# Performance work log

Hardware: AMD Instinct MI355X
Metric: run time of the kernel (lower is better)

Reference implementation:

```python
import jax, jax.numpy as jnp
import numpy as np

B, C1, C2, H, W = 8, 256, 256, 64, 64
C = 256            # int(c1*e)
G = C // 16        # 16 groups (dg)
Cg = C // G        # 16 channels per group
K = 9              # 3x3 kernel sample points
BN_EPS = 1e-5

# kernel grid offsets for 3x3, dilation 1 (pad=1 centers the grid)
KH = jnp.array([-1, -1, -1, 0, 0, 0, 1, 1, 1], jnp.float32)
KW = jnp.array([-1, 0, 1, -1, 0, 1, -1, 0, 1], jnp.float32)


def setup_inputs() -> dict:
    key = jax.random.key(0)
    ks = jax.random.split(key, 10)
    x = jax.random.normal(ks[0], (B, C1, H, W), jnp.float32)
    w_cv1 = jax.random.normal(ks[1], (C, C1), jnp.float32) / np.sqrt(C1)
    b_cv1 = jax.random.normal(ks[2], (C,), jnp.float32) * 0.1
    # offset/mask linear (DCNv4 inits to zero; small scale keeps sampling sane)
    w_off = jax.random.normal(ks[3], (G * 3 * K, C), jnp.float32) * 0.01
    b_off = jax.random.normal(ks[4], (G * 3 * K,), jnp.float32) * 0.01
    w_cv2 = jax.random.normal(ks[5], (C2, C), jnp.float32) / np.sqrt(C)
    bn_gamma = jax.random.uniform(ks[6], (C2,), jnp.float32, 0.5, 1.5)
    bn_beta = jax.random.normal(ks[7], (C2,), jnp.float32) * 0.1
    bn_mean = jax.random.normal(ks[8], (C2,), jnp.float32) * 0.1
    bn_var = jax.random.uniform(ks[9], (C2,), jnp.float32, 0.5, 1.5)
    return dict(x=x, w_cv1=w_cv1, b_cv1=b_cv1, w_off=w_off, b_off=b_off,
                w_cv2=w_cv2, bn_gamma=bn_gamma, bn_beta=bn_beta,
                bn_mean=bn_mean, bn_var=bn_var)


def _gather(vflat, hi, wi):
    # vflat: (B, H*W, G, Cg); hi/wi: (B,H,W,K,G) float corner indices
    ok = ((hi >= 0) & (hi < H) & (wi >= 0) & (wi < W)).astype(vflat.dtype)
    idx = (jnp.clip(hi, 0, H - 1) * W + jnp.clip(wi, 0, W - 1)).astype(jnp.int32)
    idx = idx.reshape(B, H * W * K, G)
    idxb = jnp.broadcast_to(idx[..., None], (B, H * W * K, G, Cg))
    g = jnp.take_along_axis(vflat, idxb, axis=1)  # (B, HWK, G, Cg)
    return g.reshape(B, H, W, K, G, Cg), ok


def _dcnv4(v, off, mask):
    # v: (B,H,W,G,Cg); off: (B,H,W,G,K,2) (dh,dw); mask: (B,H,W,G,K)
    ii = jnp.arange(H, dtype=jnp.float32)
    jj = jnp.arange(W, dtype=jnp.float32)
    ph = ii[None, :, None, None, None] + KH[None, None, None, None, :] + off[..., 0]
    pw = jj[None, None, :, None, None] + KW[None, None, None, None, :] + off[..., 1]
    ph = ph.transpose(0, 1, 2, 4, 3)  # (B,H,W,K,G)
    pw = pw.transpose(0, 1, 2, 4, 3)
    h0 = jnp.floor(ph); w0 = jnp.floor(pw)
    ah = ph - h0; aw = pw - w0
    vflat = v.reshape(B, H * W, G, Cg)
    g00, ok00 = _gather(vflat, h0, w0)
    g01, ok01 = _gather(vflat, h0, w0 + 1)
    g10, ok10 = _gather(vflat, h0 + 1, w0)
    g11, ok11 = _gather(vflat, h0 + 1, w0 + 1)
    w00 = ((1 - ah) * (1 - aw) * ok00)[..., None]
    w01 = ((1 - ah) * aw * ok01)[..., None]
    w10 = (ah * (1 - aw) * ok10)[..., None]
    w11 = (ah * aw * ok11)[..., None]
    sample = w00 * g00 + w01 * g01 + w10 * g10 + w11 * g11  # (B,H,W,K,G,Cg)
    out = jnp.einsum('bhwkgc,bhwgk->bhwgc', sample, mask)
    return out.reshape(B, H, W, C).transpose(0, 3, 1, 2)  # NCHW


def reference(x, w_cv1, b_cv1, w_off, b_off, w_cv2, bn_gamma, bn_beta, bn_mean, bn_var):
    # cv1: 1x1 conv
    h1 = jnp.einsum('bchw,oc->bohw', x, w_cv1) + b_cv1[None, :, None, None]
    # offset/mask 1x1 projection, per-group layout [2K offsets, K masks]
    om = jnp.einsum('bchw,oc->bhwo', h1, w_off) + b_off
    om = om.reshape(B, H, W, G, 3 * K)
    off = om[..., :2 * K].reshape(B, H, W, G, K, 2)
    mask = om[..., 2 * K:]  # DCNv4: no softmax, used directly
    v = h1.transpose(0, 2, 3, 1).reshape(B, H, W, G, Cg)
    y = _dcnv4(v, off, mask)
    # cv2: 1x1 conv (no bias)
    y = jnp.einsum('bchw,oc->bohw', y, w_cv2)
    # BatchNorm (eval mode)
    scale = (bn_gamma / jnp.sqrt(bn_var + BN_EPS))[None, :, None, None]
    y = (y - bn_mean[None, :, None, None]) * scale + bn_beta[None, :, None, None]
    # SiLU
    return y * jax.nn.sigmoid(y)
```

## Files before the change

kernel.cpp:

```cpp
#include <hip/hip_runtime.h>

#define HW 4096
#define CCH 256
#define MOFF 432
#define PTOT 32768

typedef unsigned short u16;
typedef __attribute__((ext_vector_type(8))) short short8;
typedef __attribute__((ext_vector_type(8))) unsigned short u16x8;
typedef __attribute__((ext_vector_type(4))) unsigned short u16x4;
typedef __attribute__((ext_vector_type(4))) float f32x4;

__device__ __forceinline__ u16 f2b(float f){
  unsigned int u = __float_as_uint(f);
  unsigned int rounding = 0x7FFFu + ((u >> 16) & 1u);
  return (u16)((u + rounding) >> 16);
}
__device__ __forceinline__ float b2f(u16 s){
  return __uint_as_float(((unsigned int)s) << 16);
}

__global__ __launch_bounds__(256) void k_cvtw(const float* __restrict__ w1,
    const float* __restrict__ woff, const float* __restrict__ w2,
    const float* __restrict__ gamma, const float* __restrict__ beta,
    const float* __restrict__ mean, const float* __restrict__ var,
    u16* __restrict__ wb1, u16* __restrict__ wboff, u16* __restrict__ wb2,
    float* __restrict__ bnA, float* __restrict__ bnB){
  int r = blockIdx.x, t = threadIdx.x;
  if (r < 256) wb1[r*256 + t] = f2b(w1[r*256 + t]);
  else if (r < 704){ int o = r - 256; wboff[o*256 + t] = (o < MOFF) ? f2b(woff[o*256 + t]) : (u16)0; }
  else if (r < 960){ int o = r - 704; wb2[o*256 + t] = f2b(w2[o*256 + t]); }
  else if (t < 256){
    float sc = gamma[t] * rsqrtf(var[t] + 1e-5f);
    bnA[t] = sc;
    bnB[t] = beta[t] - mean[t] * sc;
  }
}

__global__ __launch_bounds__(256) void k_xt(const float* __restrict__ x,
    u16* __restrict__ xT){
  __shared__ float tile[64][65];
  const int pb = blockIdx.x * 64, cb = blockIdx.y * 64, b = blockIdx.z;
  const int t = threadIdx.x;
  const float* src = x + ((size_t)(b * CCH + cb)) * HW + pb;
  #pragma unroll
  for (int pass = 0; pass < 4; ++pass){
    int c_l = pass * 16 + (t >> 4);
    int pq = (t & 15) * 4;
    float4 v = *reinterpret_cast<const float4*>(&src[(size_t)c_l * HW + pq]);
    tile[pq + 0][c_l] = v.x; tile[pq + 1][c_l] = v.y;
    tile[pq + 2][c_l] = v.z; tile[pq + 3][c_l] = v.w;
  }
  __syncthreads();
  #pragma unroll
  for (int pass = 0; pass < 4; ++pass){
    int p_l = pass * 16 + (t >> 4);
    int cq = (t & 15) * 4;
    u16x4 o4;
    #pragma unroll
    for (int j = 0; j < 4; ++j) o4[j] = f2b(tile[p_l][cq + j]);
    *reinterpret_cast<u16x4*>(&xT[((size_t)b * HW + pb + p_l) * CCH + cb + cq]) = o4;
  }
}

template<int BN, bool GUARD, bool SILU>
__global__ __launch_bounds__(256) void k_gemm(const u16* __restrict__ A,
    const u16* __restrict__ Bw, const float* __restrict__ bias,
    const float* __restrict__ bnB, void* __restrict__ Cout, int ldc, int NL){
  constexpr int WN = BN / 2;
  constexpr int MF = 4;
  constexpr int NF = WN / 16;
  constexpr int BOFF = 128 * 40;
  constexpr int STG = (128 + BN) * 40;
  constexpr int CMAT = 128 * (BN + 8);
  constexpr int SM = SILU ? STG : (STG > CMAT ? STG : CMAT);
  __shared__ __align__(16) u16 smem[SM];

  const int t = threadIdx.x;
  const int tm = blockIdx.x * 128;
  const int tn = blockIdx.y * BN;
  const int lane = t & 63;
  const int wid = t >> 6;
  const int wr = wid >> 1, wc = wid & 1;

  f32x4 acc[MF][NF] = {};

  for (int kc = 0; kc < 256; kc += 32){
    #pragma unroll
    for (int i = 0; i < 2; ++i){
      int v = t + i * 256;
      int row = v >> 2, cq = v & 3;
      *reinterpret_cast<u16x8*>(&smem[row * 40 + cq * 8]) =
        *reinterpret_cast<const u16x8*>(&A[(size_t)(tm + row) * 256 + kc + cq * 8]);
    }
    constexpr int BV = BN * 4 / 256;
    #pragma unroll
    for (int i = 0; i < BV; ++i){
      int v = t + i * 256;
      int row = v >> 2, cq = v & 3;
      *reinterpret_cast<u16x8*>(&smem[BOFF + row * 40 + cq * 8]) =
        *reinterpret_cast<const u16x8*>(&Bw[(size_t)(tn + row) * 256 + kc + cq * 8]);
    }
    __syncthreads();
    short8 af[MF], bf[NF];
    #pragma unroll
    for (int m = 0; m < MF; ++m)
      af[m] = *reinterpret_cast<const short8*>(
        &smem[(wr * 64 + m * 16 + (lane & 15)) * 40 + (lane >> 4) * 8]);
    #pragma unroll
    for (int n = 0; n < NF; ++n)
      bf[n] = *reinterpret_cast<const short8*>(
        &smem[BOFF + (wc * WN + n * 16 + (lane & 15)) * 40 + (lane >> 4) * 8]);
    #pragma unroll
    for (int m = 0; m < MF; ++m)
      #pragma unroll
      for (int n = 0; n < NF; ++n)
        acc[m][n] = __builtin_amdgcn_mfma_f32_16x16x32_bf16(af[m], bf[n], acc[m][n], 0, 0, 0);
    __syncthreads();
  }

  if constexpr (SILU){
    const int bimg = tm >> 12;
    const int ploc = tm & 4095;
    float* outp = (float*)Cout;
    #pragma unroll
    for (int n = 0; n < NF; ++n){
      int o = tn + wc * WN + n * 16 + (lane & 15);
      float sA = bias[o], sB = bnB[o];
      #pragma unroll
      for (int m = 0; m < MF; ++m){
        int prow = wr * 64 + m * 16 + ((lane >> 4) << 2);
        f32x4 st;
        #pragma unroll
        for (int j = 0; j < 4; ++j){
          float y = acc[m][n][j] * sA + sB;
          st[j] = y / (1.f + expf(-y));
        }
        *reinterpret_cast<f32x4*>(&outp[((size_t)(bimg * 256 + o)) * HW + ploc + prow]) = st;
      }
    }
  } else {
    constexpr int CP = BN + 8;
    u16* C_l = smem;
    #pragma unroll
    for (int n = 0; n < NF; ++n){
      int col = wc * WN + n * 16 + (lane & 15);
      int o = tn + col;
      float bi = (!GUARD || o < NL) ? bias[o] : 0.f;
      #pragma unroll
      for (int m = 0; m < MF; ++m){
        int r0 = wr * 64 + m * 16 + ((lane >> 4) << 2);
        #pragma unroll
        for (int j = 0; j < 4; ++j)
          C_l[(r0 + j) * CP + col] = f2b(acc[m][n][j] + bi);
      }
    }
    __syncthreads();
    constexpr int SEG = BN / 8;
    constexpr int RPP = 256 / SEG;
    u16* Co = (u16*)Cout;
    #pragma unroll
    for (int pass = 0; pass < 128 / RPP; ++pass){
      int row = pass * RPP + t / SEG;
      int sg = t % SEG;
      int oc = tn + sg * 8;
      if (!GUARD || oc + 8 <= NL)
        *reinterpret_cast<u16x8*>(&Co[(size_t)(tm + row) * ldc + oc]) =
          *reinterpret_cast<const u16x8*>(&C_l[row * CP + sg * 8]);
    }
  }
}

__global__ __launch_bounds__(256) void k_sample(const u16* __restrict__ h1n,
    const u16* __restrict__ om, u16* __restrict__ ydcn){
  __shared__ __align__(16) u16 oms[8 * MOFF];
  const int t = threadIdx.x;
  const int pblk = blockIdx.x * 8;
  {
    const u16* src = om + (size_t)pblk * MOFF;
    *reinterpret_cast<u16x8*>(&oms[t * 8]) =
      *reinterpret_cast<const u16x8*>(&src[t * 8]);
    if (t < 176)
      *reinterpret_cast<u16x8*>(&oms[(256 + t) * 8]) =
        *reinterpret_cast<const u16x8*>(&src[(256 + t) * 8]);
  }
  __syncthreads();

  const int pix = t >> 5, s = t & 31;
  const int g = s >> 1, c0 = g * 16 + (s & 1) * 8;
  const int p = pblk + pix;
  const int b = p >> 12, hw = p & 4095;
  const int ic = hw >> 6, jc = hw & 63;
  const u16* ob = &oms[pix * MOFF + g * 27];
  const u16* vb = h1n + (size_t)b * HW * CCH + c0;

  float acc[8] = {};
  #pragma unroll
  for (int k = 0; k < 9; ++k){
    float oh = b2f(ob[2 * k]);
    float ow = b2f(ob[2 * k + 1]);
    float m  = b2f(ob[18 + k]);
    float ph = (float)(ic + (k / 3) - 1) + oh;
    float pw = (float)(jc + (k % 3) - 1) + ow;
    float h0f = floorf(ph), w0f = floorf(pw);
    int h0 = (int)h0f, w0 = (int)w0f;
    float ah = ph - h0f, aw = pw - w0f;
    float cw[4];
    cw[0] = m * (1.f - ah) * (1.f - aw);
    cw[1] = m * (1.f - ah) * aw;
    cw[2] = m * ah * (1.f - aw);
    cw[3] = m * ah * aw;
    #pragma unroll
    for (int c = 0; c < 4; ++c){
      int hi = h0 + (c >> 1);
      int wi = w0 + (c & 1);
      if (hi >= 0 && hi < 64 && wi >= 0 && wi < 64){
        u16x8 val = *reinterpret_cast<const u16x8*>(&vb[(size_t)(hi * 64 + wi) * CCH]);
        float coef = cw[c];
        #pragma unroll
        for (int j = 0; j < 8; ++j) acc[j] += coef * b2f(val[j]);
      }
    }
  }
  u16x8 o8;
  #pragma unroll
  for (int j = 0; j < 8; ++j) o8[j] = f2b(acc[j]);
  *reinterpret_cast<u16x8*>(&ydcn[(size_t)p * CCH + c0]) = o8;
}

extern "C" void kernel_launch(void* const* d_in, const int* in_sizes, int n_in,
                              void* d_out, int out_size, void* d_ws, size_t ws_size,
                              hipStream_t stream) {
  const float* x     = (const float*)d_in[0];
  const float* w1    = (const float*)d_in[1];
  const float* b1    = (const float*)d_in[2];
  const float* woff  = (const float*)d_in[3];
  const float* boff  = (const float*)d_in[4];
  const float* w2    = (const float*)d_in[5];
  const float* gamma = (const float*)d_in[6];
  const float* beta  = (const float*)d_in[7];
  const float* mean  = (const float*)d_in[8];
  const float* var   = (const float*)d_in[9];
  float* out = (float*)d_out;
  (void)in_sizes; (void)n_in; (void)out_size; (void)ws_size;

  u16* h1n   = (u16*)d_ws;
  u16* om    = h1n + (size_t)PTOT * CCH;
  u16* xT    = om + (size_t)PTOT * MOFF;
  u16* ydcn  = xT;
  u16* wb1   = xT + (size_t)PTOT * CCH;
  u16* wboff = wb1 + 256 * 256;
  u16* wb2   = wboff + 448 * 256;
  float* bnA = (float*)(wb2 + 256 * 256);
  float* bnB = bnA + 256;

  dim3 blk(256);
  k_cvtw<<<dim3(961), blk, 0, stream>>>(w1, woff, w2, gamma, beta, mean, var,
                                        wb1, wboff, wb2, bnA, bnB);
  k_xt<<<dim3(64, 4, 8), blk, 0, stream>>>(x, xT);
  k_gemm<128, false, false><<<dim3(PTOT / 128, 2), blk, 0, stream>>>(
      xT, wb1, b1, nullptr, (void*)h1n, 256, 256);
  k_gemm<64, true, false><<<dim3(PTOT / 128, 7), blk, 0, stream>>>(
      h1n, wboff, boff, nullptr, (void*)om, MOFF, MOFF);
  k_sample<<<dim3(PTOT / 8), blk, 0, stream>>>(h1n, om, ydcn);
  k_gemm<128, false, true><<<dim3(PTOT / 128, 2), blk, 0, stream>>>(
      ydcn, wb2, bnA, bnB, (void*)out, 0, 256);
}
```

Measured before the change: 112.9 us.

## Fuse x transpose into cv1 GEMM, pad h1 border, widen sampler per-thread work

Removes the separate transpose kernel: the first GEMM now reads fp32 NCHW x directly, converts to bf16 and transposes into shared memory. h1 is written into a zero-bordered 66x66 padded layout, so the deformable sampler can clamp indices to the border and load all four corners unconditionally instead of branching on bounds. The sampler also handles 16 pixels per block, with one thread per group covering 16 channels, and keeps offsets in shared memory as fp32. The costs are an extra border-zeroing kernel, scattered 2-byte shared stores in the GEMM A-tile load, and more registers per sampler thread.

Measured after the change: 126.7 us. 1.12x slower.

```diff
diff --git a/kernel.cpp b/kernel.cpp
--- a/kernel.cpp
+++ b/kernel.cpp
@@ -4,11 +4,12 @@
 #define CCH 256
 #define MOFF 432
 #define PTOT 32768
+#define PDIM 66
+#define PIMG (PDIM*PDIM)
 
 typedef unsigned short u16;
 typedef __attribute__((ext_vector_type(8))) short short8;
 typedef __attribute__((ext_vector_type(8))) unsigned short u16x8;
-typedef __attribute__((ext_vector_type(4))) unsigned short u16x4;
 typedef __attribute__((ext_vector_type(4))) float f32x4;
 
 __device__ __forceinline__ u16 f2b(float f){
@@ -37,34 +38,21 @@
   }
 }
 
-__global__ __launch_bounds__(256) void k_xt(const float* __restrict__ x,
-    u16* __restrict__ xT){
-  __shared__ float tile[64][65];
-  const int pb = blockIdx.x * 64, cb = blockIdx.y * 64, b = blockIdx.z;
-  const int t = threadIdx.x;
-  const float* src = x + ((size_t)(b * CCH + cb)) * HW + pb;
-  #pragma unroll
-  for (int pass = 0; pass < 4; ++pass){
-    int c_l = pass * 16 + (t >> 4);
-    int pq = (t & 15) * 4;
-    float4 v = *reinterpret_cast<const float4*>(&src[(size_t)c_l * HW + pq]);
-    tile[pq + 0][c_l] = v.x; tile[pq + 1][c_l] = v.y;
-    tile[pq + 2][c_l] = v.z; tile[pq + 3][c_l] = v.w;
-  }
-  __syncthreads();
-  #pragma unroll
-  for (int pass = 0; pass < 4; ++pass){
-    int p_l = pass * 16 + (t >> 4);
-    int cq = (t & 15) * 4;
-    u16x4 o4;
-    #pragma unroll
-    for (int j = 0; j < 4; ++j) o4[j] = f2b(tile[p_l][cq + j]);
-    *reinterpret_cast<u16x4*>(&xT[((size_t)b * HW + pb + p_l) * CCH + cb + cq]) = o4;
-  }
-}
-
-template<int BN, bool GUARD, bool SILU>
-__global__ __launch_bounds__(256) void k_gemm(const u16* __restrict__ A,
+__global__ __launch_bounds__(256) void k_zb(u16* __restrict__ h1p){
+  int idx = blockIdx.x * 8 + (threadIdx.x >> 5);
+  int seg = threadIdx.x & 31;
+  int img = idx / 260, n = idx % 260;
+  int row, col;
+  if (n < 66){ row = 0; col = n; }
+  else if (n < 132){ row = 65; col = n - 66; }
+  else if (n < 196){ row = n - 132 + 1; col = 0; }
+  else { row = n - 196 + 1; col = 65; }
+  u16x8 z = {};
+  *reinterpret_cast<u16x8*>(&h1p[((size_t)img * PIMG + row * PDIM + col) * 256 + seg * 8]) = z;
+}
+
+template<int BN, bool GUARD, bool SILU, int AMODE, bool PADC>
+__global__ __launch_bounds__(256) void k_gemm(const void* __restrict__ Asrc,
     const u16* __restrict__ Bw, const float* __restrict__ bias,
     const float* __restrict__ bnB, void* __restrict__ Cout, int ldc, int NL){
   constexpr int WN = BN / 2;
@@ -86,12 +74,41 @@
   f32x4 acc[MF][NF] = {};
 
   for (int kc = 0; kc < 256; kc += 32){
-    #pragma unroll
-    for (int i = 0; i < 2; ++i){
-      int v = t + i * 256;
-      int row = v >> 2, cq = v & 3;
-      *reinterpret_cast<u16x8*>(&smem[row * 40 + cq * 8]) =
-        *reinterpret_cast<const u16x8*>(&A[(size_t)(tm + row) * 256 + kc + cq * 8]);
+    if constexpr (AMODE == 1){
+      const float* xs = (const float*)Asrc;
+      const int bb = tm >> 12, ploc = tm & 4095;
+      #pragma unroll
+      for (int r = 0; r < 4; ++r){
+        int flat = t + r * 256;
+        int c_l = flat >> 5, p4 = (flat & 31) * 4;
+        float4 xv = *reinterpret_cast<const float4*>(
+          &xs[((size_t)(bb * 256 + kc + c_l)) * HW + ploc + p4]);
+        smem[(p4 + 0) * 40 + c_l] = f2b(xv.x);
+        smem[(p4 + 1) * 40 + c_l] = f2b(xv.y);
+        smem[(p4 + 2) * 40 + c_l] = f2b(xv.z);
+        smem[(p4 + 3) * 40 + c_l] = f2b(xv.w);
+      }
+    } else if constexpr (AMODE == 2){
+      const u16* Ap = (const u16*)Asrc;
+      #pragma unroll
+      for (int i = 0; i < 2; ++i){
+        int v = t + i * 256;
+        int row = v >> 2, cq = v & 3;
+        int p = tm + row;
+        int bb = p >> 12, ii = (p >> 6) & 63, jj = p & 63;
+        size_t base = ((size_t)(bb * PIMG) + (ii + 1) * PDIM + jj + 1) * 256;
+        *reinterpret_cast<u16x8*>(&smem[row * 40 + cq * 8]) =
+          *reinterpret_cast<const u16x8*>(&Ap[base + kc + cq * 8]);
+      }
+    } else {
+      const u16* Ap = (const u16*)Asrc;
+      #pragma unroll
+      for (int i = 0; i < 2; ++i){
+        int v = t + i * 256;
+        int row = v >> 2, cq = v & 3;
+        *reinterpret_cast<u16x8*>(&smem[row * 40 + cq * 8]) =
+          *reinterpret_cast<const u16x8*>(&Ap[(size_t)(tm + row) * 256 + kc + cq * 8]);
+      }
     }
     constexpr int BV = BN * 4 / 256;
     #pragma unroll
@@ -164,68 +181,86 @@
       int row = pass * RPP + t / SEG;
       int sg = t % SEG;
       int oc = tn + sg * 8;
-      if (!GUARD || oc + 8 <= NL)
-        *reinterpret_cast<u16x8*>(&Co[(size_t)(tm + row) * ldc + oc]) =
+      if constexpr (PADC){
+        int p = tm + row;
+        int bb = p >> 12, ii = (p >> 6) & 63, jj = p & 63;
+        size_t dst = ((size_t)(bb * PIMG) + (ii + 1) * PDIM + jj + 1) * 256 + oc;
+        *reinterpret_cast<u16x8*>(&Co[dst]) =
           *reinterpret_cast<const u16x8*>(&C_l[row * CP + sg * 8]);
-    }
-  }
-}
-
-__global__ __launch_bounds__(256) void k_sample(const u16* __restrict__ h1n,
+      } else {
+        if (!GUARD || oc + 8 <= NL)
+          *reinterpret_cast<u16x8*>(&Co[(size_t)(tm + row) * ldc + oc]) =
+            *reinterpret_cast<const u16x8*>(&C_l[row * CP + sg * 8]);
+      }
+    }
+  }
+}
+
+__global__ __launch_bounds__(256) void k_sample(const u16* __restrict__ h1p,
     const u16* __restrict__ om, u16* __restrict__ ydcn){
-  __shared__ __align__(16) u16 oms[8 * MOFF];
+  __shared__ float oms[16 * MOFF];
   const int t = threadIdx.x;
-  const int pblk = blockIdx.x * 8;
+  const int pblk = blockIdx.x * 16;
   {
     const u16* src = om + (size_t)pblk * MOFF;
-    *reinterpret_cast<u16x8*>(&oms[t * 8]) =
-      *reinterpret_cast<const u16x8*>(&src[t * 8]);
-    if (t < 176)
-      *reinterpret_cast<u16x8*>(&oms[(256 + t) * 8]) =
-        *reinterpret_cast<const u16x8*>(&src[(256 + t) * 8]);
+    #pragma unroll
+    for (int i = 0; i < 4; ++i){
+      int idx = t + i * 256;
+      if (idx < 864){
+        u16x8 v = *reinterpret_cast<const u16x8*>(&src[idx * 8]);
+        float4 lo, hi;
+        lo.x = b2f(v[0]); lo.y = b2f(v[1]); lo.z = b2f(v[2]); lo.w = b2f(v[3]);
+        hi.x = b2f(v[4]); hi.y = b2f(v[5]); hi.z = b2f(v[6]); hi.w = b2f(v[7]);
+        *reinterpret_cast<float4*>(&oms[idx * 8]) = lo;
+        *reinterpret_cast<float4*>(&oms[idx * 8 + 4]) = hi;
+      }
+    }
   }
   __syncthreads();
-
-  const int pix = t >> 5, s = t & 31;
-  const int g = s >> 1, c0 = g * 16 + (s & 1) * 8;
+  const int pix = t >> 4, g = t & 15;
   const int p = pblk + pix;
   const int b = p >> 12, hw = p & 4095;
   const int ic = hw >> 6, jc = hw & 63;
-  const u16* ob = &oms[pix * MOFF + g * 27];
-  const u16* vb = h1n + (size_t)b * HW * CCH + c0;
-
-  float acc[8] = {};
+  const u16* vb = h1p + ((size_t)b * PIMG + PDIM + 1) * 256 + g * 16;
+  const float* ob = &oms[pix * MOFF + g * 27];
+  const float fi = (float)ic, fj = (float)jc;
+  float acc[16] = {};
   #pragma unroll
   for (int k = 0; k < 9; ++k){
-    float oh = b2f(ob[2 * k]);
-    float ow = b2f(ob[2 * k + 1]);
-    float m  = b2f(ob[18 + k]);
-    float ph = (float)(ic + (k / 3) - 1) + oh;
-    float pw = (float)(jc + (k % 3) - 1) + ow;
+    float oh = ob[2 * k], ow = ob[2 * k + 1], m = ob[18 + k];
+    float ph = fi + (float)(k / 3 - 1) + oh;
+    float pw = fj + (float)(k % 3 - 1) + ow;
     float h0f = floorf(ph), w0f = floorf(pw);
+    float ah = ph - h0f, aw = pw - w0f;
     int h0 = (int)h0f, w0 = (int)w0f;
-    float ah = ph - h0f, aw = pw - w0f;
-    float cw[4];
-    cw[0] = m * (1.f - ah) * (1.f - aw);
-    cw[1] = m * (1.f - ah) * aw;
-    cw[2] = m * ah * (1.f - aw);
-    cw[3] = m * ah * aw;
-    #pragma unroll
-    for (int c = 0; c < 4; ++c){
-      int hi = h0 + (c >> 1);
-      int wi = w0 + (c & 1);
-      if (hi >= 0 && hi < 64 && wi >= 0 && wi < 64){
-        u16x8 val = *reinterpret_cast<const u16x8*>(&vb[(size_t)(hi * 64 + wi) * CCH]);
-        float coef = cw[c];
-        #pragma unroll
-        for (int j = 0; j < 8; ++j) acc[j] += coef * b2f(val[j]);
-      }
-    }
-  }
-  u16x8 o8;
+    int h0c = min(max(h0, -1), 64), h1c = min(max(h0 + 1, -1), 64);
+    int w0c = min(max(w0, -1), 64), w1c = min(max(w0 + 1, -1), 64);
+    int r0 = h0c * PDIM, r1 = h1c * PDIM;
+    float mh1 = m * ah, mh0 = m - mh1;
+    float c01 = mh0 * aw, c00 = mh0 - c01;
+    float c11 = mh1 * aw, c10 = mh1 - c11;
+    u16x8 a00l = *reinterpret_cast<const u16x8*>(&vb[(r0 + w0c) * 256]);
+    u16x8 a00h = *reinterpret_cast<const u16x8*>(&vb[(r0 + w0c) * 256 + 8]);
+    u16x8 a01l = *reinterpret_cast<const u16x8*>(&vb[(r0 + w1c) * 256]);
+    u16x8 a01h = *reinterpret_cast<const u16x8*>(&vb[(r0 + w1c) * 256 + 8]);
+    u16x8 a10l = *reinterpret_cast<const u16x8*>(&vb[(r1 + w0c) * 256]);
+    u16x8 a10h = *reinterpret_cast<const u16x8*>(&vb[(r1 + w0c) * 256 + 8]);
+    u16x8 a11l = *reinterpret_cast<const u16x8*>(&vb[(r1 + w1c) * 256]);
+    u16x8 a11h = *reinterpret_cast<const u16x8*>(&vb[(r1 + w1c) * 256 + 8]);
+    #pragma unroll
+    for (int j = 0; j < 8; ++j){
+      acc[j]     += c00 * b2f(a00l[j]) + c01 * b2f(a01l[j])
+                  + c10 * b2f(a10l[j]) + c11 * b2f(a11l[j]);
+      acc[8 + j] += c00 * b2f(a00h[j]) + c01 * b2f(a01h[j])
+                  + c10 * b2f(a10h[j]) + c11 * b2f(a11h[j]);
+    }
+  }
+  u16x8 o0, o1;
   #pragma unroll
-  for (int j = 0; j < 8; ++j) o8[j] = f2b(acc[j]);
-  *reinterpret_cast<u16x8*>(&ydcn[(size_t)p * CCH + c0]) = o8;
+  for (int j = 0; j < 8; ++j){ o0[j] = f2b(acc[j]); o1[j] = f2b(acc[8 + j]); }
+  u16* dst = ydcn + (size_t)p * 256 + g * 16;
+  *reinterpret_cast<u16x8*>(dst) = o0;
+  *reinterpret_cast<u16x8*>(&dst[8]) = o1;
 }
 
 extern "C" void kernel_launch(void* const* d_in, const int* in_sizes, int n_in,
@@ -244,25 +279,24 @@
   float* out = (float*)d_out;
   (void)in_sizes; (void)n_in; (void)out_size; (void)ws_size;
 
-  u16* h1n   = (u16*)d_ws;
-  u16* om    = h1n + (size_t)PTOT * CCH;
-  u16* xT    = om + (size_t)PTOT * MOFF;
-  u16* ydcn  = xT;
-  u16* wb1   = xT + (size_t)PTOT * CCH;
+  u16* h1p   = (u16*)d_ws;
+  u16* om    = h1p + (size_t)8 * PIMG * 256;
+  u16* ydcn  = om + (size_t)PTOT * MOFF;
+  u16* wb1   = ydcn + (size_t)PTOT * CCH;
   u16* wboff = wb1 + 256 * 256;
   u16* wb2   = wboff + 448 * 256;
   float* bnA = (float*)(wb2 + 256 * 256);
   float* bnB = bnA + 256;
 
   dim3 blk(256);
+  k_zb  <<<dim3(260), blk, 0, stream>>>(h1p);
   k_cvtw<<<dim3(961), blk, 0, stream>>>(w1, woff, w2, gamma, beta, mean, var,
                                         wb1, wboff, wb2, bnA, bnB);
-  k_xt<<<dim3(64, 4, 8), blk, 0, stream>>>(x, xT);
-  k_gemm<128, false, false><<<dim3(PTOT / 128, 2), blk, 0, stream>>>(
-      xT, wb1, b1, nullptr, (void*)h1n, 256, 256);
-  k_gemm<64, true, false><<<dim3(PTOT / 128, 7), blk, 0, stream>>>(
-      h1n, wboff, boff, nullptr, (void*)om, MOFF, MOFF);
-  k_sample<<<dim3(PTOT / 8), blk, 0, stream>>>(h1n, om, ydcn);
-  k_gemm<128, false, true><<<dim3(PTOT / 128, 2), blk, 0, stream>>>(
-      ydcn, wb2, bnA, bnB, (void*)out, 0, 256);
-}
+  k_gemm<128, false, false, 1, true><<<dim3(PTOT / 128, 2), blk, 0, stream>>>(
+      (const void*)x, wb1, b1, nullptr, (void*)h1p, 0, 256);
+  k_gemm<64, true, false, 2, false><<<dim3(PTOT / 128, 7), blk, 0, stream>>>(
+      (const void*)h1p, wboff, boff, nullptr, (void*)om, MOFF, MOFF);
+  k_sample<<<dim3(PTOT / 16), blk, 0, stream>>>(h1p, om, ydcn);
+  k_gemm<128, false, true, 0, false><<<dim3(PTOT / 128, 2), blk, 0, stream>>>(
+      (const void*)ydcn, wb2, bnA, bnB, (void*)out, 0, 256);
+}
```

## Store h1 in zero-padded layout to remove bounds checks in deformable sampling

Applied to the files above, without the earlier changes.

The cv1 GEMM now writes h1 into a zero-bordered 68x68 per-image buffer, and the weight-conversion kernel zeroes the 2-pixel halo. The offset GEMM reads from the padded layout, and the sampler clamps corner indices into the padded range so it can issue all four bilinear loads unconditionally without per-corner branches. Offsets and masks are also unpacked to fp32 in shared memory once per block. Samples displaced further than the 2-pixel border get clamped, so equivalence with the reference rests on the offsets staying small. The layout also adds halo-zeroing writes and a larger workspace.

New measurement: 109.2 us. 1.03x faster.

```diff
diff --git a/kernel.cpp b/kernel.cpp
--- a/kernel.cpp
+++ b/kernel.cpp
@@ -4,6 +4,8 @@
 #define CCH 256
 #define MOFF 432
 #define PTOT 32768
+#define PDIM 68
+#define PIMG (PDIM*PDIM)
 
 typedef unsigned short u16;
 typedef __attribute__((ext_vector_type(8))) short short8;
@@ -25,15 +27,27 @@
     const float* __restrict__ gamma, const float* __restrict__ beta,
     const float* __restrict__ mean, const float* __restrict__ var,
     u16* __restrict__ wb1, u16* __restrict__ wboff, u16* __restrict__ wb2,
-    float* __restrict__ bnA, float* __restrict__ bnB){
+    float* __restrict__ bnA, float* __restrict__ bnB, u16* __restrict__ h1p){
   int r = blockIdx.x, t = threadIdx.x;
   if (r < 256) wb1[r*256 + t] = f2b(w1[r*256 + t]);
   else if (r < 704){ int o = r - 256; wboff[o*256 + t] = (o < MOFF) ? f2b(woff[o*256 + t]) : (u16)0; }
   else if (r < 960){ int o = r - 704; wb2[o*256 + t] = f2b(w2[o*256 + t]); }
-  else if (t < 256){
-    float sc = gamma[t] * rsqrtf(var[t] + 1e-5f);
-    bnA[t] = sc;
-    bnB[t] = beta[t] - mean[t] * sc;
+  else if (r == 960){
+    if (t < 256){
+      float sc = gamma[t] * rsqrtf(var[t] + 1e-5f);
+      bnA[t] = sc;
+      bnB[t] = beta[t] - mean[t] * sc;
+    }
+  } else {
+    int n = (r - 961) * 8 + (t >> 5);
+    int seg = t & 31;
+    int img = n / 528, m = n % 528;
+    int row, col;
+    if (m < 136){ row = m / 68; col = m % 68; }
+    else if (m < 272){ int mm = m - 136; row = 66 + mm / 68; col = mm % 68; }
+    else { int mm = m - 272; row = 2 + (mm >> 2); int c4 = mm & 3; col = (c4 & 1) + 66 * (c4 >> 1); }
+    u16x8 z = {};
+    *reinterpret_cast<u16x8*>(&h1p[((size_t)img * PIMG + row * PDIM + col) * 256 + seg * 8]) = z;
   }
 }
 
@@ -63,8 +77,8 @@
   }
 }
 
-template<int BN, bool GUARD, bool SILU>
-__global__ __launch_bounds__(256) void k_gemm(const u16* __restrict__ A,
+template<int BN, bool GUARD, bool SILU, int AMODE, bool PADC>
+__global__ __launch_bounds__(256) void k_gemm(const void* __restrict__ Asrc,
     const u16* __restrict__ Bw, const float* __restrict__ bias,
     const float* __restrict__ bnB, void* __restrict__ Cout, int ldc, int NL){
   constexpr int WN = BN / 2;
@@ -86,12 +100,27 @@
   f32x4 acc[MF][NF] = {};
 
   for (int kc = 0; kc < 256; kc += 32){
-    #pragma unroll
-    for (int i = 0; i < 2; ++i){
-      int v = t + i * 256;
-      int row = v >> 2, cq = v & 3;
-      *reinterpret_cast<u16x8*>(&smem[row * 40 + cq * 8]) =
-        *reinterpret_cast<const u16x8*>(&A[(size_t)(tm + row) * 256 + kc + cq * 8]);
+    if constexpr (AMODE == 2){
+      const u16* Ap = (const u16*)Asrc;
+      #pragma unroll
+      for (int i = 0; i < 2; ++i){
+        int v = t + i * 256;
+        int row = v >> 2, cq = v & 3;
+        int p = tm + row;
+        int bb = p >> 12, ii = (p >> 6) & 63, jj = p & 63;
+        size_t base = ((size_t)(bb * PIMG) + (ii + 2) * PDIM + jj + 2) * 256;
+        *reinterpret_cast<u16x8*>(&smem[row * 40 + cq * 8]) =
+          *reinterpret_cast<const u16x8*>(&Ap[base + kc + cq * 8]);
+      }
+    } else {
+      const u16* Ap = (const u16*)Asrc;
+      #pragma unroll
+      for (int i = 0; i < 2; ++i){
+        int v = t + i * 256;
+        int row = v >> 2, cq = v & 3;
+        *reinterpret_cast<u16x8*>(&smem[row * 40 + cq * 8]) =
+          *reinterpret_cast<const u16x8*>(&Ap[(size_t)(tm + row) * 256 + kc + cq * 8]);
+      }
     }
     constexpr int BV = BN * 4 / 256;
     #pragma unroll
@@ -164,68 +193,82 @@
       int row = pass * RPP + t / SEG;
       int sg = t % SEG;
       int oc = tn + sg * 8;
-      if (!GUARD || oc + 8 <= NL)
-        *reinterpret_cast<u16x8*>(&Co[(size_t)(tm + row) * ldc + oc]) =
+      if constexpr (PADC){
+        int p = tm + row;
+        int bb = p >> 12, ii = (p >> 6) & 63, jj = p & 63;
+        size_t dst = ((size_t)(bb * PIMG) + (ii + 2) * PDIM + jj + 2) * 256 + oc;
+        *reinterpret_cast<u16x8*>(&Co[dst]) =
           *reinterpret_cast<const u16x8*>(&C_l[row * CP + sg * 8]);
-    }
-  }
-}
-
-__global__ __launch_bounds__(256) void k_sample(const u16* __restrict__ h1n,
+      } else {
+        if (!GUARD || oc + 8 <= NL)
+          *reinterpret_cast<u16x8*>(&Co[(size_t)(tm + row) * ldc + oc]) =
+            *reinterpret_cast<const u16x8*>(&C_l[row * CP + sg * 8]);
+      }
+    }
+  }
+}
+
+__global__ __launch_bounds__(256) void k_sample(const u16* __restrict__ h1p,
     const u16* __restrict__ om, u16* __restrict__ ydcn){
-  __shared__ __align__(16) u16 oms[8 * MOFF];
+  __shared__ float oms[8 * MOFF];
   const int t = threadIdx.x;
   const int pblk = blockIdx.x * 8;
   {
     const u16* src = om + (size_t)pblk * MOFF;
-    *reinterpret_cast<u16x8*>(&oms[t * 8]) =
-      *reinterpret_cast<const u16x8*>(&src[t * 8]);
-    if (t < 176)
-      *reinterpret_cast<u16x8*>(&oms[(256 + t) * 8]) =
-        *reinterpret_cast<const u16x8*>(&src[(256 + t) * 8]);
+    #pragma unroll
+    for (int i = 0; i < 2; ++i){
+      int idx = t + i * 256;
+      if (idx < 432){
+        u16x8 v = *reinterpret_cast<const u16x8*>(&src[idx * 8]);
+        float4 lo, hi;
+        lo.x = b2f(v[0]); lo.y = b2f(v[1]); lo.z = b2f(v[2]); lo.w = b2f(v[3]);
+        hi.x = b2f(v[4]); hi.y = b2f(v[5]); hi.z = b2f(v[6]); hi.w = b2f(v[7]);
+        *reinterpret_cast<float4*>(&oms[idx * 8]) = lo;
+        *reinterpret_cast<float4*>(&oms[idx * 8 + 4]) = hi;
+      }
+    }
   }
   __syncthreads();
 
   const int pix = t >> 5, s = t & 31;
-  const int g = s >> 1, c0 = g * 16 + (s & 1) * 8;
+  const int g = s >> 1, half = s & 1;
   const int p = pblk + pix;
   const int b = p >> 12, hw = p & 4095;
   const int ic = hw >> 6, jc = hw & 63;
-  const u16* ob = &oms[pix * MOFF + g * 27];
-  const u16* vb = h1n + (size_t)b * HW * CCH + c0;
+  const u16* vb = h1p + (size_t)b * PIMG * 256 + g * 16 + half * 8;
+  const float* ob = &oms[pix * MOFF + g * 27];
+  const float fi = (float)ic, fj = (float)jc;
 
   float acc[8] = {};
   #pragma unroll
   for (int k = 0; k < 9; ++k){
-    float oh = b2f(ob[2 * k]);
-    float ow = b2f(ob[2 * k + 1]);
-    float m  = b2f(ob[18 + k]);
-    float ph = (float)(ic + (k / 3) - 1) + oh;
-    float pw = (float)(jc + (k % 3) - 1) + ow;
+    float oh = ob[2 * k], ow = ob[2 * k + 1], m = ob[18 + k];
+    float ph = fi + (float)(k / 3 - 1) + oh;
+    float pw = fj + (float)(k % 3 - 1) + ow;
     float h0f = floorf(ph), w0f = floorf(pw);
+    float ah = ph - h0f, aw = pw - w0f;
     int h0 = (int)h0f, w0 = (int)w0f;
-    float ah = ph - h0f, aw = pw - w0f;
-    float cw[4];
-    cw[0] = m * (1.f - ah) * (1.f - aw);
-    cw[1] = m * (1.f - ah) * aw;
-    cw[2] = m * ah * (1.f - aw);
-    cw[3] = m * ah * aw;
-    #pragma unroll
-    for (int c = 0; c < 4; ++c){
-      int hi = h0 + (c >> 1);
-      int wi = w0 + (c & 1);
-      if (hi >= 0 && hi < 64 && wi >= 0 && wi < 64){
-        u16x8 val = *reinterpret_cast<const u16x8*>(&vb[(size_t)(hi * 64 + wi) * CCH]);
-        float coef = cw[c];
-        #pragma unroll
-        for (int j = 0; j < 8; ++j) acc[j] += coef * b2f(val[j]);
-      }
+    int hc = min(max(h0, -2), 64) + 2;
+    int wc = min(max(w0, -2), 64) + 2;
+    const u16* c0 = &vb[(hc * PDIM + wc) * 256];
+    const u16* c1 = c0 + PDIM * 256;
+    float mh1 = m * ah, mh0 = m - mh1;
+    float c01w = mh0 * aw, c00w = mh0 - c01w;
+    float c11w = mh1 * aw, c10w = mh1 - c11w;
+    u16x8 a00 = *reinterpret_cast<const u16x8*>(c0);
+    u16x8 a01 = *reinterpret_cast<const u16x8*>(c0 + 256);
+    u16x8 a10 = *reinterpret_cast<const u16x8*>(c1);
+    u16x8 a11 = *reinterpret_cast<const u16x8*>(c1 + 256);
+    #pragma unroll
+    for (int j = 0; j < 8; ++j){
+      acc[j] += c00w * b2f(a00[j]) + c01w * b2f(a01[j])
+              + c10w * b2f(a10[j]) + c11w * b2f(a11[j]);
     }
   }
   u16x8 o8;
   #pragma unroll
   for (int j = 0; j < 8; ++j) o8[j] = f2b(acc[j]);
-  *reinterpret_cast<u16x8*>(&ydcn[(size_t)p * CCH + c0]) = o8;
+  *reinterpret_cast<u16x8*>(&ydcn[(size_t)p * 256 + g * 16 + half * 8]) = o8;
 }
 
 extern "C" void kernel_launch(void* const* d_in, const int* in_sizes, int n_in,
@@ -244,8 +287,8 @@
   float* out = (float*)d_out;
   (void)in_sizes; (void)n_in; (void)out_size; (void)ws_size;
 
-  u16* h1n   = (u16*)d_ws;
-  u16* om    = h1n + (size_t)PTOT * CCH;
+  u16* h1p   = (u16*)d_ws;
+  u16* om    = h1p + (size_t)8 * PIMG * 256;
   u16* xT    = om + (size_t)PTOT * MOFF;
   u16* ydcn  = xT;
   u16* wb1   = xT + (size_t)PTOT * CCH;
@@ -255,14 +298,14 @@
   float* bnB = bnA + 256;
 
   dim3 blk(256);
-  k_cvtw<<<dim3(961), blk, 0, stream>>>(w1, woff, w2, gamma, beta, mean, var,
-                                        wb1, wboff, wb2, bnA, bnB);
+  k_cvtw<<<dim3(1489), blk, 0, stream>>>(w1, woff, w2, gamma, beta, mean, var,
+                                         wb1, wboff, wb2, bnA, bnB, h1p);
   k_xt<<<dim3(64, 4, 8), blk, 0, stream>>>(x, xT);
-  k_gemm<128, false, false><<<dim3(PTOT / 128, 2), blk, 0, stream>>>(
-      xT, wb1, b1, nullptr, (void*)h1n, 256, 256);
-  k_gemm<64, true, false><<<dim3(PTOT / 128, 7), blk, 0, stream>>>(
-      h1n, wboff, boff, nullptr, (void*)om, MOFF, MOFF);
-  k_sample<<<dim3(PTOT / 8), blk, 0, stream>>>(h1n, om, ydcn);
-  k_gemm<128, false, true><<<dim3(PTOT / 128, 2), blk, 0, stream>>>(
-      ydcn, wb2, bnA, bnB, (void*)out, 0, 256);
-}
+  k_gemm<128, false, false, 0, true><<<dim3(PTOT / 128, 2), blk, 0, stream>>>(
+      (const void*)xT, wb1, b1, nullptr, (void*)h1p, 0, 256);
+  k_gemm<64, true, false, 2, false><<<dim3(PTOT / 128, 7), blk, 0, stream>>>(
+      (const void*)h1p, wboff, boff, nullptr, (void*)om, MOFF, MOFF);
+  k_sample<<<dim3(PTOT / 8), blk, 0, stream>>>(h1p, om, ydcn);
+  k_gemm<128, false, true, 0, false><<<dim3(PTOT / 128, 2), blk, 0, stream>>>(
+      (const void*)ydcn, wb2, bnA, bnB, (void*)out, 0, 256);
+}
```
